# Kernel tuning notes

Hardware: AMD Instinct MI355X
Metric: run time of the kernel (lower is better)

## Reference

```python
import jax, jax.numpy as jnp
import numpy as np

B, N, DM, H, FF = 8, 2048, 1024, 16, 4096
D = DM // H // 2  # head_dim = 32
LAMBDA_INIT = 0.8 - 0.6 * float(np.exp(-0.3 * 1.0))  # layer_num=1


def _layernorm(x, g, b, eps=1e-5):
    mu = jnp.mean(x, axis=-1, keepdims=True)
    var = jnp.mean(jnp.square(x - mu), axis=-1, keepdims=True)
    return (x - mu) * jax.lax.rsqrt(var + eps) * g + b


def _rmsnorm(x, eps=1e-5):
    return x * jax.lax.rsqrt(jnp.mean(x * x, axis=-1, keepdims=True) + eps)


def _diff_attn(x, Wq, Wk, Wv, lq1, lq2, lk1, lk2, Wo, bo):
    b, n, d = x.shape
    scale = D ** -0.5
    # rearrange 'b n (h d q) -> b n (q h) d'
    q = (x @ Wq.T).reshape(b, n, H, D, 2).transpose(0, 1, 4, 2, 3).reshape(b, n, 2 * H, D) * scale
    k = (x @ Wk.T).reshape(b, n, H, D, 2).transpose(0, 1, 4, 2, 3).reshape(b, n, 2 * H, D)
    # rearrange 'b n (h d) -> b h n d' with d = 2*head_dim
    v = (x @ Wv.T).reshape(b, n, H, 2 * D).transpose(0, 2, 1, 3)
    # per-position head-vs-head scores: [b, n, 2H, 2H]
    att = jnp.einsum('bnqd,bnkd->bnqk', q, k)
    att = jnp.nan_to_num(att)
    att = jax.nn.softmax(att.astype(jnp.float32), axis=-1)
    lam = jnp.exp(jnp.sum(lq1 * lk1)) - jnp.exp(jnp.sum(lq2 * lk2)) + LAMBDA_INIT
    # rearrange 'b n (q h) (k a) -> q k b n h a'; take [0,0] - lam*[1,1]
    att6 = att.reshape(b, n, 2, H, 2, H)
    att2 = att6[:, :, 0, :, 0, :] - lam * att6[:, :, 1, :, 1, :]  # [b,n,h,a]
    out = jnp.einsum('bnah,bhnd->bnad', att2, v)  # [b,n,H,2D]
    out = _rmsnorm(out) * (1.0 - LAMBDA_INIT)
    out = out.reshape(b, n, d)
    return out @ Wo.T + bo


def setup_inputs() -> dict:
    key = jax.random.key(0)
    ks = jax.random.split(key, 12)
    p = lambda k, sh, s=0.02: jax.random.normal(k, sh, jnp.float32) * s
    return {
        'x': jax.random.normal(ks[0], (B, N, DM), jnp.float32),
        'Wq': p(ks[1], (DM, DM)), 'Wk': p(ks[2], (DM, DM)), 'Wv': p(ks[3], (DM, DM)),
        'lq1': p(ks[4], (D,), 0.1), 'lq2': p(ks[5], (D,), 0.1),
        'lk1': p(ks[6], (D,), 0.1), 'lk2': p(ks[7], (D,), 0.1),
        'Wo': p(ks[8], (DM, DM)), 'bo': jnp.zeros((DM,), jnp.float32),
        'ln1_g': jnp.ones((DM,), jnp.float32), 'ln1_b': jnp.zeros((DM,), jnp.float32),
        'ln2_g': jnp.ones((DM,), jnp.float32), 'ln2_b': jnp.zeros((DM,), jnp.float32),
        'W1': p(ks[9], (FF, DM)), 'b1': jnp.zeros((FF,), jnp.float32),
        'W2': p(ks[10], (DM, FF)), 'b2': jnp.zeros((DM,), jnp.float32),
    }


def reference(x, Wq, Wk, Wv, lq1, lq2, lk1, lk2, Wo, bo, ln1_g, ln1_b, ln2_g, ln2_b, W1, b1, W2, b2):
    # norm_first=True, use_gate=False, dropout=0 (eval), wo_ffn=False
    skip = x
    h = _layernorm(x, ln1_g, ln1_b)
    src2 = _diff_attn(h, Wq, Wk, Wv, lq1, lq2, lk1, lk2, Wo, bo)
    conn = skip + src2
    skip2 = conn
    h2 = _layernorm(conn, ln2_g, ln2_b)
    src3 = jax.nn.relu(h2 @ W1.T + b1) @ W2.T + b2
    return skip2 + src3
```

## Files before the change

### kernel.cpp

```cpp
#include <hip/hip_runtime.h>
#include <cstdint>

#define DM    1024
#define NHEAD 16
#define FFDIM 4096
#define MROWS 16384

static constexpr float LAMBDA_INIT_F = 0.3555090675909693f;
static constexpr float ONE_MINUS_LI  = 1.0f - 0.3555090675909693f;
static constexpr float QSCALE        = 0.17677669529663687f;

typedef __attribute__((ext_vector_type(8))) short bf16x8;
typedef __attribute__((ext_vector_type(4))) float f32x4;

__device__ __forceinline__ unsigned short f2bf(float f) {
    union { float f; unsigned int i; } w; w.f = f;
    unsigned int x = w.i;
    return (unsigned short)((x + 0x7fffu + ((x >> 16) & 1u)) >> 16);
}
__device__ __forceinline__ float bf2f(unsigned short u) {
    union { unsigned int i; float f; } w; w.i = ((unsigned int)u) << 16; return w.f;
}

__device__ __forceinline__ void load_lds16(const void* gptr, void* lptr) {
    __builtin_amdgcn_global_load_lds(
        (const __attribute__((address_space(1))) unsigned int*)gptr,
        (__attribute__((address_space(3))) unsigned int*)lptr, 16, 0, 0);
}

__global__ __launch_bounds__(256) void cvt6_kernel(const float* __restrict__ Wq,
                                                   const float* __restrict__ Wk,
                                                   const float* __restrict__ Wv,
                                                   const float* __restrict__ Wo,
                                                   const float* __restrict__ W1,
                                                   const float* __restrict__ W2,
                                                   unsigned short* __restrict__ wqkv,
                                                   unsigned short* __restrict__ wo,
                                                   unsigned short* __restrict__ w1,
                                                   unsigned short* __restrict__ w2)
{
    const int b = blockIdx.x;
    const float* src;
    unsigned short* dst;
    int off;
    if (b < 3072)      { src = (b < 1024) ? Wq : (b < 2048) ? Wk : Wv;
                         dst = wqkv + (b >> 10) * (DM * DM);
                         off = (b & 1023) * 1024; }
    else if (b < 4096) { src = Wo; dst = wo; off = (b - 3072) * 1024; }
    else if (b < 8192) { src = W1; dst = w1; off = (b - 4096) * 1024; }
    else               { src = W2; dst = w2; off = (b - 8192) * 1024; }
    const int i = off + threadIdx.x * 4;
    const float4 v = *(const float4*)&src[i];
    ushort4 o;
    o.x = f2bf(v.x); o.y = f2bf(v.y); o.z = f2bf(v.z); o.w = f2bf(v.w);
    *(ushort4*)&dst[i] = o;
}

__global__ __launch_bounds__(256) void ln_kernel(const float* __restrict__ xin,
                                                 const float* __restrict__ g,
                                                 const float* __restrict__ b,
                                                 unsigned short* __restrict__ out)
{
    const int row = blockIdx.x;
    const int tid = threadIdx.x;
    const float* xr = xin + (size_t)row * DM;
    float v[4];
    #pragma unroll
    for (int i = 0; i < 4; ++i) v[i] = xr[tid + 256 * i];
    float s1 = v[0] + v[1] + v[2] + v[3];
    float s2 = v[0]*v[0] + v[1]*v[1] + v[2]*v[2] + v[3]*v[3];
    #pragma unroll
    for (int off = 32; off > 0; off >>= 1) {
        s1 += __shfl_down(s1, off);
        s2 += __shfl_down(s2, off);
    }
    __shared__ float red[8];
    const int wv = tid >> 6;
    if ((tid & 63) == 0) { red[wv] = s1; red[4 + wv] = s2; }
    __syncthreads();
    s1 = red[0] + red[1] + red[2] + red[3];
    s2 = red[4] + red[5] + red[6] + red[7];
    const float mean = s1 * (1.0f / DM);
    const float var  = s2 * (1.0f / DM) - mean * mean;
    const float inv  = rsqrtf(var + 1e-5f);
    #pragma unroll
    for (int i = 0; i < 4; ++i) {
        const int c = tid + 256 * i;
        out[(size_t)row * DM + c] = f2bf((v[i] - mean) * inv * g[c] + b[c]);
    }
}

template<int EPI>
__global__ __launch_bounds__(256) void gemm_bt(const unsigned short* __restrict__ A,
                                               const unsigned short* __restrict__ W,
                                               void* __restrict__ Cout,
                                               const float* __restrict__ bias,
                                               const float* __restrict__ resid,
                                               int M, int N, int K)
{
    constexpr int BM = 128, BN = 128, BK = 64;
    constexpr int G = BK / 8;
    __shared__ __align__(16) unsigned short Alds[BM * BK];
    __shared__ __align__(16) unsigned short Blds[BN * BK];

    const int tid  = threadIdx.x;
    const int lane = tid & 63;
    const int wave = tid >> 6;
    const int l15  = lane & 15;
    const int q4   = lane >> 4;
    const int m0   = blockIdx.y * BM;
    const int n0   = blockIdx.x * BN;
    const int wm   = (wave >> 1) * 64;
    const int wn   = (wave & 1) * 64;

    const f32x4 fzero = {0.f, 0.f, 0.f, 0.f};
    f32x4 acc[4][4];
    #pragma unroll
    for (int i = 0; i < 4; ++i)
        #pragma unroll
        for (int j = 0; j < 4; ++j) acc[i][j] = fzero;

    const int rL  = lane >> 3;
    const int gsw = (lane & 7) ^ (rL & (G-1));
    const unsigned short* ga = A + (size_t)(m0 + wave * 32 + rL) * K + gsw * 8;
    const unsigned short* gb = W + (size_t)(n0 + wave * 32 + rL) * K + gsw * 8;
    unsigned short* la0 = &Alds[wave * 32 * BK];
    unsigned short* lb0 = &Blds[wave * 32 * BK];

    const int sa = q4 ^ (l15 & 7);

    for (int k0 = 0; k0 < K; k0 += BK) {
        #pragma unroll
        for (int c = 0; c < 4; ++c) {
            load_lds16(ga + (size_t)(c * 8) * K, la0 + c * 8 * BK);
            load_lds16(gb + (size_t)(c * 8) * K, lb0 + c * 8 * BK);
        }
        ga += BK; gb += BK;
        __syncthreads();
        #pragma unroll
        for (int kk = 0; kk < 2; ++kk) {
            const int goff = ((kk == 0) ? sa : (sa ^ 4)) * 8;
            bf16x8 af[4], bfr[4];
            #pragma unroll
            for (int i = 0; i < 4; ++i) af[i]  = *(const bf16x8*)&Alds[(wm + i * 16 + l15) * BK + goff];
            #pragma unroll
            for (int j = 0; j < 4; ++j) bfr[j] = *(const bf16x8*)&Blds[(wn + j * 16 + l15) * BK + goff];
            #pragma unroll
            for (int i = 0; i < 4; ++i)
                #pragma unroll
                for (int j = 0; j < 4; ++j)
                    acc[i][j] = __builtin_amdgcn_mfma_f32_16x16x32_bf16(af[i], bfr[j], acc[i][j], 0, 0, 0);
        }
        __syncthreads();
    }

    #pragma unroll
    for (int i = 0; i < 4; ++i) {
        #pragma unroll
        for (int j = 0; j < 4; ++j) {
            #pragma unroll
            for (int r = 0; r < 4; ++r) {
                const int m = m0 + wm + i * 16 + q4 * 4 + r;
                const int n = n0 + wn + j * 16 + l15;
                const size_t off = (size_t)m * N + n;
                float c = acc[i][j][r];
                if (EPI == 0) {
                    ((unsigned short*)Cout)[off] = f2bf(c);
                } else if (EPI == 1) {
                    c += bias[n] + resid[off];
                    ((float*)Cout)[off] = c;
                } else if (EPI == 2) {
                    c += bias[n];
                    c = fmaxf(c, 0.f);
                    ((unsigned short*)Cout)[off] = f2bf(c);
                } else {
                    c += bias[n] + resid[off];
                    ((float*)Cout)[off] = c;
                }
            }
        }
    }
}

#define QKVS 3072
__global__ __launch_bounds__(256) void attn_pos(const unsigned short* __restrict__ qkv,
                                                const float* __restrict__ lq1,
                                                const float* __restrict__ lq2,
                                                const float* __restrict__ lk1,
                                                const float* __restrict__ lk2,
                                                unsigned short* __restrict__ outg)
{
    __shared__ __align__(16) float q2[4][32][36];
    __shared__ __align__(16) float k2[4][32][36];
    __shared__ __align__(16) float v2[4][16][64];
    __shared__ float att2[4][16][17];

    const int tid  = threadIdx.x;
    const int wave = tid >> 6;
    const int lane = tid & 63;
    const int pos  = blockIdx.x * 4 + wave;

    float s1 = 0.f, s2 = 0.f;
    #pragma unroll
    for (int i = 0; i < 32; ++i) {
        s1 += lq1[i] * lk1[i];
        s2 += lq2[i] * lk2[i];
    }
    const float lam = __expf(s1) - __expf(s2) + LAMBDA_INIT_F;

    const unsigned short* qrow = qkv + (size_t)pos * QKVS;
    const unsigned short* krow = qrow + DM;
    const unsigned short* vrow = qrow + 2 * DM;

    unsigned short tq[16], tk[16], tv[16];
    *(uint4*)&tq[0] = *(const uint4*)&qrow[lane * 16];
    *(uint4*)&tq[8] = *(const uint4*)&qrow[lane * 16 + 8];
    *(uint4*)&tk[0] = *(const uint4*)&krow[lane * 16];
    *(uint4*)&tk[8] = *(const uint4*)&krow[lane * 16 + 8];
    *(uint4*)&tv[0] = *(const uint4*)&vrow[lane * 16];
    *(uint4*)&tv[8] = *(const uint4*)&vrow[lane * 16 + 8];

    #pragma unroll
    for (int jj = 0; jj < 16; ++jj) {
        const int c  = lane * 16 + jj;
        const int h  = c >> 6;
        const int d  = (c >> 1) & 31;
        const int qi = c & 1;
        q2[wave][qi * 16 + h][d] = bf2f(tq[jj]) * QSCALE;
        k2[wave][qi * 16 + h][d] = bf2f(tk[jj]);
        v2[wave][c >> 6][c & 63] = bf2f(tv[jj]);
    }
    __syncthreads();

    const int qh = lane & 31, half = lane >> 5;
    float qreg[32];
    #pragma unroll
    for (int d4 = 0; d4 < 32; d4 += 4) {
        const f32x4 t = *(const f32x4*)&q2[wave][qh][d4];
        qreg[d4] = t[0]; qreg[d4+1] = t[1]; qreg[d4+2] = t[2]; qreg[d4+3] = t[3];
    }
    float p[16];
    #pragma unroll
    for (int jj = 0; jj < 16; ++jj) {
        const float* kr = &k2[wave][half * 16 + jj][0];
        float a = 0.f;
        #pragma unroll
        for (int d4 = 0; d4 < 32; d4 += 4) {
            const f32x4 kv = *(const f32x4*)&kr[d4];
            a += qreg[d4]*kv[0] + qreg[d4+1]*kv[1] + qreg[d4+2]*kv[2] + qreg[d4+3]*kv[3];
        }
        p[jj] = a;
    }

    float mx = p[0];
    #pragma unroll
    for (int jj = 1; jj < 16; ++jj) mx = fmaxf(mx, p[jj]);
    mx = fmaxf(mx, __shfl_xor(mx, 32));
    float sum = 0.f;
    #pragma unroll
    for (int jj = 0; jj < 16; ++jj) { p[jj] = __expf(p[jj] - mx); sum += p[jj]; }
    sum += __shfl_xor(sum, 32);
    const float inv = 1.0f / sum;

    if (half == 0 && qh < 16) {
        #pragma unroll
        for (int jj = 0; jj < 16; ++jj) att2[wave][qh][jj] = p[jj] * inv;
    }
    __syncthreads();
    if (half == 1 && qh >= 16) {
        const int a = qh - 16;
        #pragma unroll
        for (int jj = 0; jj < 16; ++jj) att2[wave][a][jj] -= lam * p[jj] * inv;
    }
    __syncthreads();

    const int a   = lane & 15;
    const int ddb = (lane >> 4) * 16;
    float areg[16];
    #pragma unroll
    for (int h = 0; h < 16; ++h) areg[h] = att2[wave][a][h];
    float o[16];
    #pragma unroll
    for (int j = 0; j < 16; ++j) o[j] = 0.f;
    #pragma unroll
    for (int h = 0; h < 16; ++h) {
        #pragma unroll
        for (int j4 = 0; j4 < 16; j4 += 4) {
            const f32x4 vv = *(const f32x4*)&v2[wave][h][ddb + j4];
            o[j4]   += areg[h] * vv[0];
            o[j4+1] += areg[h] * vv[1];
            o[j4+2] += areg[h] * vv[2];
            o[j4+3] += areg[h] * vv[3];
        }
    }

    float ss = 0.f;
    #pragma unroll
    for (int j = 0; j < 16; ++j) ss += o[j] * o[j];
    ss += __shfl_xor(ss, 16);
    ss += __shfl_xor(ss, 32);
    const float scl = rsqrtf(ss * (1.0f / 64.0f) + 1e-5f) * ONE_MINUS_LI;

    unsigned short ob[16];
    #pragma unroll
    for (int j = 0; j < 16; ++j) ob[j] = f2bf(o[j] * scl);
    unsigned short* orow = outg + (size_t)pos * DM + a * 64 + ddb;
    *(uint4*)&orow[0] = *(const uint4*)&ob[0];
    *(uint4*)&orow[8] = *(const uint4*)&ob[8];
}

extern "C" void kernel_launch(void* const* d_in, const int* in_sizes, int n_in,
                              void* d_out, int out_size, void* d_ws, size_t ws_size,
                              hipStream_t stream)
{
    const float* x   = (const float*)d_in[0];
    const float* Wq  = (const float*)d_in[1];
    const float* Wk  = (const float*)d_in[2];
    const float* Wv  = (const float*)d_in[3];
    const float* lq1 = (const float*)d_in[4];
    const float* lq2 = (const float*)d_in[5];
    const float* lk1 = (const float*)d_in[6];
    const float* lk2 = (const float*)d_in[7];
    const float* Wo  = (const float*)d_in[8];
    const float* bo  = (const float*)d_in[9];
    const float* g1  = (const float*)d_in[10];
    const float* be1 = (const float*)d_in[11];
    const float* g2  = (const float*)d_in[12];
    const float* be2 = (const float*)d_in[13];
    const float* W1  = (const float*)d_in[14];
    const float* b1  = (const float*)d_in[15];
    const float* W2  = (const float*)d_in[16];
    const float* b2  = (const float*)d_in[17];
    (void)in_sizes; (void)n_in; (void)out_size;

    const size_t MB = 1ull << 20;
    char* ws = (char*)d_ws;
    unsigned short* wqkv = (unsigned short*)(ws);
    unsigned short* wo   = (unsigned short*)(ws + 6 * MB);
    unsigned short* w1   = (unsigned short*)(ws + 8 * MB);
    unsigned short* w2   = (unsigned short*)(ws + 16 * MB);
    unsigned short* h    = (unsigned short*)(ws + 24 * MB);
    unsigned short* qkv  = (unsigned short*)(ws + 56 * MB);
    float*          conn = (float*)(ws + 56 * MB);
    unsigned short* attn = h;
    unsigned short* h2   = (unsigned short*)(ws + 120 * MB);
    unsigned short* t    = (unsigned short*)(ws + 152 * MB);

    int nch = 1;
    while (nch < 128 && 152 * MB + (size_t)(MROWS / nch) * FFDIM * 2 > ws_size) nch <<= 1;
    const int MC = MROWS / nch;

    const dim3 blk(256);

    cvt6_kernel<<<12288, blk, 0, stream>>>(Wq, Wk, Wv, Wo, W1, W2, wqkv, wo, w1, w2);

    ln_kernel<<<MROWS, blk, 0, stream>>>(x, g1, be1, h);

    gemm_bt<0><<<dim3(QKVS / 128, MROWS / 128), blk, 0, stream>>>(
        h, wqkv, qkv, nullptr, nullptr, MROWS, QKVS, DM);

    attn_pos<<<MROWS / 4, blk, 0, stream>>>(qkv, lq1, lq2, lk1, lk2, attn);

    gemm_bt<1><<<dim3(DM / 128, MROWS / 128), blk, 0, stream>>>(
        attn, wo, conn, bo, x, MROWS, DM, DM);

    ln_kernel<<<MROWS, blk, 0, stream>>>(conn, g2, be2, h2);

    for (int c = 0; c < nch; ++c) {
        const size_t roff = (size_t)c * MC;
        gemm_bt<2><<<dim3(FFDIM / 128, MC / 128), blk, 0, stream>>>(
            h2 + roff * DM, w1, t, b1, nullptr, MC, FFDIM, DM);
        gemm_bt<3><<<dim3(DM / 128, MC / 128), blk, 0, stream>>>(
            t, w2, (float*)d_out + roff * DM, b2, conn + roff * DM, MC, DM, FFDIM);
    }
}
```

Before: 827.5 us.

## Replace 128x128 GEMM with 256x256 double-buffered ping-pong MFMA kernel

Swaps the 128x128 single-buffered GEMM for a 256x256-tile, 512-thread kernel. It double-buffers A and B in LDS, interleaves staged global-to-LDS loads with MFMA phases, and uses explicit barriers, waitcnt and setprio. The FFN is now chunked along the FF dimension rather than along rows, accumulating partial W2 products into the output through a residual epilogue. The goal is more data reuse per tile and better overlap of memory with compute. The cost is heavier LDS and register use and fragile hand-written synchronisation.

```diff
diff --git a/kernel.cpp b/kernel.cpp
--- a/kernel.cpp
+++ b/kernel.cpp
@@ -5,6 +5,7 @@
 #define NHEAD 16
 #define FFDIM 4096
 #define MROWS 16384
+#define QKVS  3072
 
 static constexpr float LAMBDA_INIT_F = 0.3555090675909693f;
 static constexpr float ONE_MINUS_LI  = 1.0f - 0.3555090675909693f;
@@ -91,98 +92,196 @@
 }
 
 template<int EPI>
-__global__ __launch_bounds__(256) void gemm_bt(const unsigned short* __restrict__ A,
-                                               const unsigned short* __restrict__ W,
-                                               void* __restrict__ Cout,
-                                               const float* __restrict__ bias,
-                                               const float* __restrict__ resid,
-                                               int M, int N, int K)
+__global__ __launch_bounds__(512, 2) void gemm256(const unsigned short* __restrict__ A,
+                                                  const unsigned short* __restrict__ W,
+                                                  void* __restrict__ Cout,
+                                                  const float* __restrict__ bias,
+                                                  const float* __restrict__ resid,
+                                                  int M, int N, int K, int ldb)
 {
-    constexpr int BM = 128, BN = 128, BK = 64;
-    constexpr int G = BK / 8;
-    __shared__ __align__(16) unsigned short Alds[BM * BK];
-    __shared__ __align__(16) unsigned short Blds[BN * BK];
+    __shared__ __align__(16) unsigned short Al[2][256][64];
+    __shared__ __align__(16) unsigned short Bl[2][256][64];
 
     const int tid  = threadIdx.x;
     const int lane = tid & 63;
-    const int wave = tid >> 6;
+    const int wv   = tid >> 6;
     const int l15  = lane & 15;
     const int q4   = lane >> 4;
-    const int m0   = blockIdx.y * BM;
-    const int n0   = blockIdx.x * BN;
-    const int wm   = (wave >> 1) * 64;
-    const int wn   = (wave & 1) * 64;
-
-    const f32x4 fzero = {0.f, 0.f, 0.f, 0.f};
-    f32x4 acc[4][4];
-    #pragma unroll
-    for (int i = 0; i < 4; ++i)
-        #pragma unroll
-        for (int j = 0; j < 4; ++j) acc[i][j] = fzero;
-
-    const int rL  = lane >> 3;
-    const int gsw = (lane & 7) ^ (rL & (G-1));
-    const unsigned short* ga = A + (size_t)(m0 + wave * 32 + rL) * K + gsw * 8;
-    const unsigned short* gb = W + (size_t)(n0 + wave * 32 + rL) * K + gsw * 8;
-    unsigned short* la0 = &Alds[wave * 32 * BK];
-    unsigned short* lb0 = &Blds[wave * 32 * BK];
-
-    const int sa = q4 ^ (l15 & 7);
-
-    for (int k0 = 0; k0 < K; k0 += BK) {
-        #pragma unroll
-        for (int c = 0; c < 4; ++c) {
-            load_lds16(ga + (size_t)(c * 8) * K, la0 + c * 8 * BK);
-            load_lds16(gb + (size_t)(c * 8) * K, lb0 + c * 8 * BK);
-        }
-        ga += BK; gb += BK;
-        __syncthreads();
-        #pragma unroll
-        for (int kk = 0; kk < 2; ++kk) {
-            const int goff = ((kk == 0) ? sa : (sa ^ 4)) * 8;
-            bf16x8 af[4], bfr[4];
+    const int wg   = wv >> 2;
+    const int cg   = wv & 3;
+    const int m0   = blockIdx.y * 256;
+    const int n0   = blockIdx.x * 256;
+    const int KT   = K >> 6;
+
+    const int sr = tid >> 3;
+    const int sc = (tid & 7) ^ (sr & 7);
+    const unsigned short* gA = A + (size_t)(m0 + sr) * K   + sc * 8;
+    const unsigned short* gB = W + (size_t)(n0 + sr) * ldb + sc * 8;
+    const size_t aH = (size_t)128 * K;
+    const size_t bH = (size_t)128 * ldb;
+    const size_t aC = (size_t)64 * K;
+    const size_t bC = (size_t)64 * ldb;
+    unsigned short* lA = &Al[0][0][0] + wv * 512;
+    unsigned short* lB = &Bl[0][0][0] + wv * 512;
+
+#define STG_A(boff, hoff, gp) do { \
+    load_lds16((gp),      lA + (boff) + (hoff)); \
+    load_lds16((gp) + aC, lA + (boff) + (hoff) + 4096); } while (0)
+#define STG_B(boff, hoff, gp) do { \
+    load_lds16((gp),      lB + (boff) + (hoff)); \
+    load_lds16((gp) + bC, lB + (boff) + (hoff) + 4096); } while (0)
+
+    STG_A(0, 0,    gA);
+    STG_B(0, 0,    gB);
+    STG_A(0, 8192, gA + aH);
+    STG_B(0, 8192, gB + bH);
+    if (KT > 1) {
+        STG_A(16384, 0,    gA + 64);
+        STG_B(16384, 0,    gB + 64);
+        STG_A(16384, 8192, gA + aH + 64);
+        asm volatile("s_waitcnt vmcnt(6)" ::: "memory");
+    } else {
+        asm volatile("s_waitcnt vmcnt(0)" ::: "memory");
+    }
+    __builtin_amdgcn_s_barrier();
+    __builtin_amdgcn_sched_barrier(0);
+
+    const int so0 = ( q4      ^ (l15 & 7)) * 8;
+    const int so1 = ((q4 + 4) ^ (l15 & 7)) * 8;
+    const unsigned short* rA = &Al[0][wg * 64 + l15][0];
+    const unsigned short* rB = &Bl[0][cg * 32 + l15][0];
+
+    const f32x4 fz = {0.f, 0.f, 0.f, 0.f};
+    f32x4 acc[8][4];
+    #pragma unroll
+    for (int i = 0; i < 8; ++i)
+        #pragma unroll
+        for (int j = 0; j < 4; ++j) acc[i][j] = fz;
+
+    bf16x8 a[4][2], b0[2][2], b1[2][2];
+
+    for (int t = 0; t < KT; ++t) {
+        const int bo = (t & 1) << 14;
+        const int bn = bo ^ 16384;
+        const int k1 = (t + 1) << 6;
+        const int k2 = (t + 2) << 6;
+
+        #pragma unroll
+        for (int mf = 0; mf < 4; ++mf) {
+            a[mf][0] = *(const bf16x8*)&rA[bo + mf * 1024 + so0];
+            a[mf][1] = *(const bf16x8*)&rA[bo + mf * 1024 + so1];
+        }
+        #pragma unroll
+        for (int nf = 0; nf < 2; ++nf) {
+            b0[nf][0] = *(const bf16x8*)&rB[bo + nf * 1024 + so0];
+            b0[nf][1] = *(const bf16x8*)&rB[bo + nf * 1024 + so1];
+        }
+        if (t + 1 < KT) STG_B(bn, 8192, gB + bH + k1);
+        __builtin_amdgcn_s_barrier();
+        __builtin_amdgcn_sched_barrier(0);
+        __builtin_amdgcn_s_setprio(1);
+        #pragma unroll
+        for (int mf = 0; mf < 4; ++mf)
             #pragma unroll
-            for (int i = 0; i < 4; ++i) af[i]  = *(const bf16x8*)&Alds[(wm + i * 16 + l15) * BK + goff];
+            for (int nf = 0; nf < 2; ++nf) {
+                acc[mf][nf] = __builtin_amdgcn_mfma_f32_16x16x32_bf16(a[mf][0], b0[nf][0], acc[mf][nf], 0, 0, 0);
+                acc[mf][nf] = __builtin_amdgcn_mfma_f32_16x16x32_bf16(a[mf][1], b0[nf][1], acc[mf][nf], 0, 0, 0);
+            }
+        __builtin_amdgcn_s_setprio(0);
+        __builtin_amdgcn_s_barrier();
+        __builtin_amdgcn_sched_barrier(0);
+
+        #pragma unroll
+        for (int nf = 0; nf < 2; ++nf) {
+            b1[nf][0] = *(const bf16x8*)&rB[bo + 8192 + nf * 1024 + so0];
+            b1[nf][1] = *(const bf16x8*)&rB[bo + 8192 + nf * 1024 + so1];
+        }
+        if (t + 2 < KT) STG_A(bo, 0, gA + k2);
+        __builtin_amdgcn_s_barrier();
+        __builtin_amdgcn_sched_barrier(0);
+        __builtin_amdgcn_s_setprio(1);
+        #pragma unroll
+        for (int mf = 0; mf < 4; ++mf)
             #pragma unroll
-            for (int j = 0; j < 4; ++j) bfr[j] = *(const bf16x8*)&Blds[(wn + j * 16 + l15) * BK + goff];
+            for (int nf = 0; nf < 2; ++nf) {
+                acc[mf][2 + nf] = __builtin_amdgcn_mfma_f32_16x16x32_bf16(a[mf][0], b1[nf][0], acc[mf][2 + nf], 0, 0, 0);
+                acc[mf][2 + nf] = __builtin_amdgcn_mfma_f32_16x16x32_bf16(a[mf][1], b1[nf][1], acc[mf][2 + nf], 0, 0, 0);
+            }
+        __builtin_amdgcn_s_setprio(0);
+        __builtin_amdgcn_s_barrier();
+        __builtin_amdgcn_sched_barrier(0);
+
+        #pragma unroll
+        for (int mf = 0; mf < 4; ++mf) {
+            a[mf][0] = *(const bf16x8*)&rA[bo + 8192 + mf * 1024 + so0];
+            a[mf][1] = *(const bf16x8*)&rA[bo + 8192 + mf * 1024 + so1];
+        }
+        if (t + 2 < KT) STG_B(bo, 0, gB + k2);
+        __builtin_amdgcn_s_barrier();
+        __builtin_amdgcn_sched_barrier(0);
+        __builtin_amdgcn_s_setprio(1);
+        #pragma unroll
+        for (int mf = 0; mf < 4; ++mf)
             #pragma unroll
-            for (int i = 0; i < 4; ++i)
-                #pragma unroll
-                for (int j = 0; j < 4; ++j)
-                    acc[i][j] = __builtin_amdgcn_mfma_f32_16x16x32_bf16(af[i], bfr[j], acc[i][j], 0, 0, 0);
-        }
-        __syncthreads();
-    }
-
-    #pragma unroll
-    for (int i = 0; i < 4; ++i) {
-        #pragma unroll
-        for (int j = 0; j < 4; ++j) {
+            for (int nf = 0; nf < 2; ++nf) {
+                acc[4 + mf][nf] = __builtin_amdgcn_mfma_f32_16x16x32_bf16(a[mf][0], b0[nf][0], acc[4 + mf][nf], 0, 0, 0);
+                acc[4 + mf][nf] = __builtin_amdgcn_mfma_f32_16x16x32_bf16(a[mf][1], b0[nf][1], acc[4 + mf][nf], 0, 0, 0);
+            }
+        __builtin_amdgcn_s_setprio(0);
+        __builtin_amdgcn_s_barrier();
+        __builtin_amdgcn_sched_barrier(0);
+
+        if (t + 2 < KT) STG_A(bo, 8192, gA + aH + k2);
+        __builtin_amdgcn_s_barrier();
+        __builtin_amdgcn_sched_barrier(0);
+        __builtin_amdgcn_s_setprio(1);
+        #pragma unroll
+        for (int mf = 0; mf < 4; ++mf)
             #pragma unroll
-            for (int r = 0; r < 4; ++r) {
-                const int m = m0 + wm + i * 16 + q4 * 4 + r;
-                const int n = n0 + wn + j * 16 + l15;
-                const size_t off = (size_t)m * N + n;
-                float c = acc[i][j][r];
-                if (EPI == 0) {
-                    ((unsigned short*)Cout)[off] = f2bf(c);
-                } else if (EPI == 1) {
-                    c += bias[n] + resid[off];
-                    ((float*)Cout)[off] = c;
-                } else if (EPI == 2) {
-                    c += bias[n];
-                    c = fmaxf(c, 0.f);
-                    ((unsigned short*)Cout)[off] = f2bf(c);
-                } else {
-                    c += bias[n] + resid[off];
-                    ((float*)Cout)[off] = c;
-                }
+            for (int nf = 0; nf < 2; ++nf) {
+                acc[4 + mf][2 + nf] = __builtin_amdgcn_mfma_f32_16x16x32_bf16(a[mf][0], b1[nf][0], acc[4 + mf][2 + nf], 0, 0, 0);
+                acc[4 + mf][2 + nf] = __builtin_amdgcn_mfma_f32_16x16x32_bf16(a[mf][1], b1[nf][1], acc[4 + mf][2 + nf], 0, 0, 0);
             }
-        }
-    }
-}
-
-#define QKVS 3072
+        __builtin_amdgcn_s_setprio(0);
+        if (t + 2 < KT) {
+            asm volatile("s_waitcnt vmcnt(6)" ::: "memory");
+        } else if (t + 2 == KT) {
+            asm volatile("s_waitcnt vmcnt(0)" ::: "memory");
+        }
+        if (t + 1 < KT) {
+            __builtin_amdgcn_s_barrier();
+            __builtin_amdgcn_sched_barrier(0);
+        }
+    }
+#undef STG_A
+#undef STG_B
+
+    #pragma unroll
+    for (int hm = 0; hm < 2; ++hm)
+    #pragma unroll
+    for (int mf = 0; mf < 4; ++mf)
+    #pragma unroll
+    for (int hb = 0; hb < 2; ++hb)
+    #pragma unroll
+    for (int nf = 0; nf < 2; ++nf)
+    #pragma unroll
+    for (int rr = 0; rr < 4; ++rr) {
+        const int m = m0 + hm * 128 + wg * 64 + mf * 16 + q4 * 4 + rr;
+        const int n = n0 + hb * 128 + cg * 32 + nf * 16 + l15;
+        const size_t off = (size_t)m * N + n;
+        float c = acc[hm * 4 + mf][hb * 2 + nf][rr];
+        if (EPI == 0) {
+            ((unsigned short*)Cout)[off] = f2bf(c);
+        } else if (EPI == 1) {
+            ((float*)Cout)[off] = c + bias[n] + resid[off];
+        } else if (EPI == 2) {
+            ((unsigned short*)Cout)[off] = f2bf(fmaxf(c + bias[n], 0.f));
+        } else {
+            ((float*)Cout)[off] = c + resid[off];
+        }
+    }
+}
+
 __global__ __launch_bounds__(256) void attn_pos(const unsigned short* __restrict__ qkv,
                                                 const float* __restrict__ lq1,
                                                 const float* __restrict__ lq2,
@@ -346,31 +445,34 @@
     unsigned short* h2   = (unsigned short*)(ws + 120 * MB);
     unsigned short* t    = (unsigned short*)(ws + 152 * MB);
 
-    int nch = 1;
-    while (nch < 128 && 152 * MB + (size_t)(MROWS / nch) * FFDIM * 2 > ws_size) nch <<= 1;
-    const int MC = MROWS / nch;
-
-    const dim3 blk(256);
-
-    cvt6_kernel<<<12288, blk, 0, stream>>>(Wq, Wk, Wv, Wo, W1, W2, wqkv, wo, w1, w2);
-
-    ln_kernel<<<MROWS, blk, 0, stream>>>(x, g1, be1, h);
-
-    gemm_bt<0><<<dim3(QKVS / 128, MROWS / 128), blk, 0, stream>>>(
-        h, wqkv, qkv, nullptr, nullptr, MROWS, QKVS, DM);
-
-    attn_pos<<<MROWS / 4, blk, 0, stream>>>(qkv, lq1, lq2, lk1, lk2, attn);
-
-    gemm_bt<1><<<dim3(DM / 128, MROWS / 128), blk, 0, stream>>>(
-        attn, wo, conn, bo, x, MROWS, DM, DM);
-
-    ln_kernel<<<MROWS, blk, 0, stream>>>(conn, g2, be2, h2);
-
-    for (int c = 0; c < nch; ++c) {
-        const size_t roff = (size_t)c * MC;
-        gemm_bt<2><<<dim3(FFDIM / 128, MC / 128), blk, 0, stream>>>(
-            h2 + roff * DM, w1, t, b1, nullptr, MC, FFDIM, DM);
-        gemm_bt<3><<<dim3(DM / 128, MC / 128), blk, 0, stream>>>(
-            t, w2, (float*)d_out + roff * DM, b2, conn + roff * DM, MC, DM, FFDIM);
-    }
-}
+    int nf = 1;
+    while (nf < 16 && 152 * MB + (size_t)MROWS * (FFDIM / nf) * 2 > ws_size) nf <<= 1;
+    const int FC = FFDIM / nf;
+
+    const dim3 b256(256), b512(512);
+
+    cvt6_kernel<<<12288, b256, 0, stream>>>(Wq, Wk, Wv, Wo, W1, W2, wqkv, wo, w1, w2);
+
+    ln_kernel<<<MROWS, b256, 0, stream>>>(x, g1, be1, h);
+
+    gemm256<0><<<dim3(QKVS / 256, MROWS / 256), b512, 0, stream>>>(
+        h, wqkv, qkv, nullptr, nullptr, MROWS, QKVS, DM, DM);
+
+    attn_pos<<<MROWS / 4, b256, 0, stream>>>(qkv, lq1, lq2, lk1, lk2, attn);
+
+    gemm256<1><<<dim3(DM / 256, MROWS / 256), b512, 0, stream>>>(
+        attn, wo, conn, bo, x, MROWS, DM, DM, DM);
+
+    ln_kernel<<<MROWS, b256, 0, stream>>>(conn, g2, be2, h2);
+
+    for (int c = 0; c < nf; ++c) {
+        gemm256<2><<<dim3(FC / 256, MROWS / 256), b512, 0, stream>>>(
+            h2, w1 + (size_t)c * FC * DM, t, b1 + c * FC, nullptr, MROWS, FC, DM, DM);
+        if (c == 0)
+            gemm256<1><<<dim3(DM / 256, MROWS / 256), b512, 0, stream>>>(
+                t, w2 + (size_t)c * FC, (float*)d_out, b2, conn, MROWS, DM, FC, FFDIM);
+        else
+            gemm256<4><<<dim3(DM / 256, MROWS / 256), b512, 0, stream>>>(
+                t, w2 + (size_t)c * FC, (float*)d_out, nullptr, (const float*)d_out, MROWS, DM, FC, FFDIM);
+    }
+}
```

Result: faster. 707.8 us (-14.5%).
